# Kernel optimization log

Measured on AMD Instinct MI355X. Metric: run time of the kernel, lower is better.

The kernel has to match this reference:

```python
import jax, jax.numpy as jnp
import numpy as np

B, N = 65536, 8
OBS0, OBS1, OBS2 = 6, 1024, 7
H, HC, NA = 64, 128, 2


def _glorot(key, shape):
    fan_in = shape[0]
    lim = 1.0 / np.sqrt(fan_in)
    return jax.random.uniform(key, shape, jnp.float32, -lim, lim)


def setup_inputs() -> dict:
    key = jax.random.key(0)
    ks = jax.random.split(key, 24)
    state0 = jax.random.normal(ks[0], (B, OBS0), jnp.float32)
    state1 = jax.random.normal(ks[1], (B, OBS1), jnp.float32)
    state2 = jax.random.normal(ks[2], (B, N, OBS2), jnp.float32)
    keep = (jax.random.uniform(ks[3], (B, N, 1)) > 0.35) | (jnp.arange(N)[None, :, None] == 0)
    state2 = state2 * keep.astype(jnp.float32)
    return {
        "state0": state0, "state1": state1, "state2": state2,
        "W0": _glorot(ks[4], (OBS0, H)), "b0": jnp.zeros((H,), jnp.float32),
        "Wg": _glorot(ks[5], (OBS1, H)), "bg": jnp.zeros((H,), jnp.float32),
        "Ws1": _glorot(ks[6], (OBS2, H)), "bs1": jnp.zeros((H,), jnp.float32),
        "Ws2": _glorot(ks[7], (H, H)), "bs2": jnp.zeros((H,), jnp.float32),
        "Wq": _glorot(ks[8], (H, H)),
        "Wk": _glorot(ks[9], (H, H)),
        "Wv": _glorot(ks[10], (H, H)),
        "Wc1": _glorot(ks[11], (3 * H, HC)), "bc1": jnp.zeros((HC,), jnp.float32),
        "Wc2": _glorot(ks[12], (HC, HC)), "bc2": jnp.zeros((HC,), jnp.float32),
        "Wc3": _glorot(ks[13], (HC, NA)), "bc3": jnp.zeros((NA,), jnp.float32),
    }


def reference(state0, state1, state2,
              W0, b0, Wg, bg, Ws1, bs1, Ws2, bs2,
              Wq, Wk, Wv, Wc1, bc1, Wc2, bc2, Wc3, bc3):
    own_e = jax.nn.relu(state0 @ W0 + b0)                      # [B, 64]
    env_e = jax.nn.relu(state1 @ Wg + bg)                      # [B, 64]
    intru_e = jax.nn.relu(state2 @ Ws1 + bs1)                  # [B, N, 64]
    intru_e = jax.nn.relu(intru_e @ Ws2 + bs2)                 # [B, N, 64]

    q = own_e @ Wq                                             # [B, 64]
    k = intru_e @ Wk                                           # [B, N, 64]
    v = intru_e @ Wv                                           # [B, N, 64]

    # mask: True where the neighbor slot is non-padding (mean over feats != 0)
    mask = jnp.mean(state2, axis=2, keepdims=True) != 0        # [B, N, 1] bool

    score = jnp.einsum('bnd,bd->bn', k, q)[..., None]          # [B, N, 1]
    score_m = jnp.where(mask, score, -jnp.inf)
    alpha = jax.nn.softmax(score_m / np.sqrt(H), axis=1)       # [B, N, 1]
    alpha_m = jnp.where(mask, alpha, 0.0)
    v_att = jnp.sum(v * alpha_m, axis=1)                       # [B, 64]

    concat = jnp.concatenate((own_e, env_e, v_att), axis=1)    # [B, 192]
    h = jax.nn.relu(concat @ Wc1 + bc1)
    h = jax.nn.relu(h @ Wc2 + bc2)
    return jnp.tanh(h @ Wc3 + bc3)                             # [B, n_actions]
```

## Files before the change

kernel.cpp:

```cpp
#include <hip/hip_runtime.h>
#include <math.h>


typedef float f32x4 __attribute__((ext_vector_type(4)));
typedef float f32x4u __attribute__((ext_vector_type(4), aligned(4)));
typedef float f32x2u __attribute__((ext_vector_type(2), aligned(4)));
typedef __bf16 bf16x8 __attribute__((ext_vector_type(8)));
typedef unsigned short u16x8 __attribute__((ext_vector_type(8)));

#define DI __device__ __forceinline__

DI unsigned short f2bf_u(float f) {
  unsigned u = __builtin_bit_cast(unsigned, f);
  u += 0x7fffu + ((u >> 16) & 1u);
  return (unsigned short)(u >> 16);
}
DI float bfu2f(unsigned short s) {
  unsigned u = ((unsigned)s) << 16;
  return __builtin_bit_cast(float, u);
}
DI u16x8 cvt8(f32x4 x, f32x4 y) {
  bf16x8 r;
  r[0] = (__bf16)x[0]; r[1] = (__bf16)x[1]; r[2] = (__bf16)x[2]; r[3] = (__bf16)x[3];
  r[4] = (__bf16)y[0]; r[5] = (__bf16)y[1]; r[6] = (__bf16)y[2]; r[7] = (__bf16)y[3];
  return __builtin_bit_cast(u16x8, r);
}
DI f32x4 mfma16(u16x8 a, u16x8 b, f32x4 c) {
  return __builtin_amdgcn_mfma_f32_16x16x32_bf16(
      __builtin_bit_cast(bf16x8, a), __builtin_bit_cast(bf16x8, b), c, 0, 0, 0);
}


constexpr size_t WS_WGF = 0;
constexpr size_t WS_WS2 = 131072;
constexpr size_t WS_WV  = 139264;
constexpr size_t WS_MQK = 147456;
constexpr size_t WS_WC1 = 155648;
constexpr size_t WS_WC2 = 204800;
constexpr size_t WS_ENV = 237568;

__global__ __launch_bounds__(256) void k_prep(
    const float* __restrict__ Wg, const float* __restrict__ Ws2,
    const float* __restrict__ Wv, const float* __restrict__ Wq,
    const float* __restrict__ Wk, const float* __restrict__ Wc1,
    const float* __restrict__ Wc2,
    unsigned short* __restrict__ wgf, unsigned short* __restrict__ ws2f,
    unsigned short* __restrict__ wvf, unsigned short* __restrict__ mqkf,
    unsigned short* __restrict__ wc1f, unsigned short* __restrict__ wc2f) {
  const int idx = blockIdx.x * 256 + threadIdx.x;
  const float* src = nullptr;
  unsigned short* dst;
  int i, ntm, NC;
  bool is_mqk = false;
  if (idx < 65536)      { src = Wg;  dst = wgf;  i = idx;          ntm = 2; NC = 64;  }
  else if (idx < 69632) { src = Ws2; dst = ws2f; i = idx - 65536;  ntm = 2; NC = 64;  }
  else if (idx < 73728) { src = Wv;  dst = wvf;  i = idx - 69632;  ntm = 2; NC = 64;  }
  else if (idx < 77824) { is_mqk = true; dst = mqkf; i = idx - 73728; ntm = 2; NC = 64; }
  else if (idx < 102400){ src = Wc1; dst = wc1f; i = idx - 77824;  ntm = 3; NC = 128; }
  else                  { src = Wc2; dst = wc2f; i = idx - 102400; ntm = 3; NC = 128; }
  const int j = i & 7, ln = (i >> 3) & 63, t2 = i >> 9;
  const int nt = t2 & ((1 << ntm) - 1), kt = t2 >> ntm;
  const int k = kt * 32 + (ln >> 4) * 8 + j, n = nt * 16 + (ln & 15);
  float val;
  if (is_mqk) {
    const f32x4* qp = (const f32x4*)(Wq + k * 64);
    const f32x4* kp = (const f32x4*)(Wk + n * 64);
    float acc = 0.f;
#pragma unroll
    for (int d4 = 0; d4 < 16; ++d4) {
      const f32x4 a = qp[d4], b = kp[d4];
#pragma unroll
      for (int e = 0; e < 4; ++e) acc = fmaf(a[e], b[e], acc);
    }
    val = acc;
  } else {
    val = src[k * NC + n];
  }
  dst[i] = f2bf_u(val);
}

__global__ __launch_bounds__(256, 3) void k_env(
    const float* __restrict__ s1, const float* __restrict__ bg,
    const unsigned short* __restrict__ wgf, unsigned short* __restrict__ env) {
  __shared__ __align__(16) f32x4 RED[16 * 64];
  const int tid = threadIdx.x, lane = tid & 63, wave = tid >> 6;
  const int lo = lane & 15, q = lane >> 4;
  const int r0 = blockIdx.x * 16;
  const float* arow = s1 + (size_t)(r0 + lo) * 1024 + wave * 256 + q * 8;

  f32x4 A[8][2];
#pragma unroll
  for (int ks = 0; ks < 8; ++ks) {
    A[ks][0] = *(const f32x4*)(arow + ks * 32);
    A[ks][1] = *(const f32x4*)(arow + ks * 32 + 4);
  }
  const u16x8* wp = (const u16x8*)wgf + lane;
  u16x8 Bb[2][4];
#pragma unroll
  for (int nt = 0; nt < 4; ++nt) Bb[0][nt] = wp[((wave * 8) * 4 + nt) * 64];
  f32x4 acc[4] = {};
#pragma unroll
  for (int ks = 0; ks < 8; ++ks) {
    const int cur = ks & 1;
    if (ks < 7) {
#pragma unroll
      for (int nt = 0; nt < 4; ++nt)
        Bb[cur ^ 1][nt] = wp[((wave * 8 + ks + 1) * 4 + nt) * 64];
    }
    const u16x8 af = cvt8(A[ks][0], A[ks][1]);
#pragma unroll
    for (int nt = 0; nt < 4; ++nt) acc[nt] = mfma16(af, Bb[cur][nt], acc[nt]);
  }
#pragma unroll
  for (int nt = 0; nt < 4; ++nt) RED[(wave * 4 + nt) * 64 + lane] = acc[nt];
  __syncthreads();
  f32x4 s = RED[(0 * 4 + wave) * 64 + lane];
#pragma unroll
  for (int p = 1; p < 4; ++p) s += RED[(p * 4 + wave) * 64 + lane];
  const float bias = bg[wave * 16 + lo];
#pragma unroll
  for (int ri = 0; ri < 4; ++ri)
    env[(size_t)(r0 + q * 4 + ri) * 64 + wave * 16 + lo] =
        f2bf_u(fmaxf(s[ri] + bias, 0.f));
}

__global__ __launch_bounds__(256, 3) void k_rest(
    const float* __restrict__ s0, const float* __restrict__ s2,
    const unsigned short* __restrict__ env,
    const float* __restrict__ W0, const float* __restrict__ b0v,
    const float* __restrict__ Ws1, const float* __restrict__ bs1,
    const unsigned short* __restrict__ ws2f, const float* __restrict__ bs2,
    const unsigned short* __restrict__ wvf, const unsigned short* __restrict__ mqkf,
    const unsigned short* __restrict__ wc1f, const float* __restrict__ bc1,
    const unsigned short* __restrict__ wc2f, const float* __restrict__ bc2,
    const float* __restrict__ Wc3, const float* __restrict__ bc3,
    float* __restrict__ out) {
  __shared__ __align__(16) char smem[53248];
  u16x8* EF = (u16x8*)smem;
  unsigned short* EFs = (unsigned short*)smem;
  u16x8* H1F = (u16x8*)smem;
  unsigned short* H1Fs = (unsigned short*)smem;
  float* H2 = (float*)(smem + 8192);
  u16x8* CF = (u16x8*)(smem + 32768);
  unsigned short* CFs = (unsigned short*)(smem + 32768);
  float* SC = (float*)(smem + 36864);
  float* QK = (float*)(smem + 45056);
  u16x8* SEF = (u16x8*)(smem + 45056);

  const int tid = threadIdx.x;
  const int lane = tid & 63, wave = tid >> 6;
  const int lo = lane & 15, q = lane >> 4;
  const int bbase = blockIdx.x * 32;

  const int bl8 = tid >> 3, n8 = tid & 7;
  const float* s2p = s2 + ((size_t)(bbase + bl8) * 8 + n8) * 7;
  const f32x4u x03 = *(const f32x4u*)s2p;
  const f32x2u x45 = *(const f32x2u*)(s2p + 4);
  const float x6 = s2p[6];
  const float* s0p = s0 + (size_t)(bbase + bl8) * 6;
  const f32x4u y03 = *(const f32x4u*)s0p;
  const f32x2u y45 = *(const f32x2u*)(s0p + 4);
  const u16x8 ev = *(const u16x8*)(env + (size_t)(bbase + bl8) * 64 + n8 * 8);

  bool maskreg;
  {
    float xv[7] = {x03[0], x03[1], x03[2], x03[3], x45[0], x45[1], x6};
    const float sum = xv[0] + xv[1] + xv[2] + xv[3] + xv[4] + xv[5] + xv[6];
    maskreg = (sum != 0.f);
    const int mt = tid >> 4, rl = tid & 15;
#pragma unroll
    for (int c = 0; c < 8; ++c) {
      float a[8];
#pragma unroll
      for (int i = 0; i < 8; ++i) a[i] = bs1[c * 8 + i];
#pragma unroll
      for (int j = 0; j < 7; ++j) {
        const float* wr = Ws1 + j * 64 + c * 8;
#pragma unroll
        for (int i = 0; i < 8; ++i) a[i] = fmaf(xv[j], wr[i], a[i]);
      }
      u16x8 pk;
#pragma unroll
      for (int i = 0; i < 8; ++i) pk[i] = f2bf_u(fmaxf(a[i], 0.f));
      EF[(mt * 2 + (c >> 2)) * 64 + (((c & 3) << 4) | rl)] = pk;
    }
  }
  __syncthreads();

  {
    u16x8 Bf[4][2];
#pragma unroll
    for (int nt = 0; nt < 4; ++nt)
#pragma unroll
      for (int kt = 0; kt < 2; ++kt)
        Bf[nt][kt] = ((const u16x8*)ws2f)[(kt * 4 + nt) * 64 + lane];
    float bias[4];
#pragma unroll
    for (int nt = 0; nt < 4; ++nt) bias[nt] = bs2[nt * 16 + lo];
#pragma unroll
    for (int mi = 0; mi < 4; ++mi) {
      const int mt = wave * 4 + mi;
      const u16x8 A0 = EF[(mt * 2 + 0) * 64 + lane];
      const u16x8 A1 = EF[(mt * 2 + 1) * 64 + lane];
      f32x4 acc[4] = {};
#pragma unroll
      for (int nt = 0; nt < 4; ++nt) {
        acc[nt] = mfma16(A0, Bf[nt][0], acc[nt]);
        acc[nt] = mfma16(A1, Bf[nt][1], acc[nt]);
      }
#pragma unroll
      for (int nt = 0; nt < 4; ++nt) {
        const int h = nt * 16 + lo;
#pragma unroll
        for (int ri = 0; ri < 4; ++ri) {
          const float v = fmaxf(acc[nt][ri] + bias[nt], 0.f);
          const int rr = mt * 16 + q * 4 + ri;
          EFs[((mt * 2 + (h >> 5)) * 64 + ((((h >> 3) & 3) << 4) | (rr & 15))) * 8 +
              (h & 7)] = f2bf_u(v);
        }
      }
    }
  }
  __syncthreads();

  {
    const int mt = bl8 >> 4, fl = ((n8 & 3) << 4) | (bl8 & 15), kt = n8 >> 2;
    const float yv[6] = {y03[0], y03[1], y03[2], y03[3], y45[0], y45[1]};
    float a[8];
#pragma unroll
    for (int i = 0; i < 8; ++i) a[i] = b0v[n8 * 8 + i];
#pragma unroll
    for (int j = 0; j < 6; ++j) {
      const float* wr = W0 + j * 64 + n8 * 8;
#pragma unroll
      for (int i = 0; i < 8; ++i) a[i] = fmaf(yv[j], wr[i], a[i]);
    }
    u16x8 pk;
#pragma unroll
    for (int i = 0; i < 8; ++i) pk[i] = f2bf_u(fmaxf(a[i], 0.f));
    CF[(mt * 6 + kt) * 64 + fl] = pk;
    CF[(mt * 6 + 2 + kt) * 64 + fl] = ev;
  }
  __syncthreads();

  {
#pragma unroll
    for (int pp = 0; pp < 2; ++pp) {
      const int pr = wave * 2 + pp, mt = pr >> 2, nt = pr & 3;
      const u16x8 A0 = CF[(mt * 6 + 0) * 64 + lane];
      const u16x8 A1 = CF[(mt * 6 + 1) * 64 + lane];
      const u16x8 B0 = ((const u16x8*)mqkf)[(0 * 4 + nt) * 64 + lane];
      const u16x8 B1 = ((const u16x8*)mqkf)[(1 * 4 + nt) * 64 + lane];
      f32x4 acc = {};
      acc = mfma16(A0, B0, acc);
      acc = mfma16(A1, B1, acc);
#pragma unroll
      for (int ri = 0; ri < 4; ++ri)
        QK[(mt * 16 + q * 4 + ri) * 64 + nt * 16 + lo] = acc[ri];
    }
  }
  __syncthreads();

  {
    const int r = tid, bl = r >> 3, mt = r >> 4, rl = r & 15;
    float dot = 0.f;
#pragma unroll
    for (int c = 0; c < 8; ++c) {
      const u16x8 e = EF[(mt * 2 + (c >> 2)) * 64 + (((c & 3) << 4) | rl)];
      const float* qkp = QK + bl * 64 + c * 8;
      const f32x4 qa = *(const f32x4*)(qkp);
      const f32x4 qb = *(const f32x4*)(qkp + 4);
#pragma unroll
      for (int i = 0; i < 4; ++i) dot = fmaf(bfu2f(e[i]), qa[i], dot);
#pragma unroll
      for (int i = 0; i < 4; ++i) dot = fmaf(bfu2f(e[4 + i]), qb[i], dot);
    }
    SC[r] = maskreg ? dot * 0.125f : -1e30f;
  }
  __syncthreads();

  if (tid < 32) {
    float s[8];
#pragma unroll
    for (int n = 0; n < 8; ++n) s[n] = SC[tid * 8 + n];
    float mx = s[0];
#pragma unroll
    for (int n = 1; n < 8; ++n) mx = fmaxf(mx, s[n]);
    float e[8], sum = 0.f;
#pragma unroll
    for (int n = 0; n < 8; ++n) { e[n] = __expf(s[n] - mx); sum += e[n]; }
    const float inv = 1.f / sum;
#pragma unroll
    for (int n = 0; n < 8; ++n) SC[tid * 8 + n] = e[n] * inv;
  }
  __syncthreads();

  {
    float al[8];
#pragma unroll
    for (int n = 0; n < 8; ++n) al[n] = SC[bl8 * 8 + n];
    float a[8] = {0.f, 0.f, 0.f, 0.f, 0.f, 0.f, 0.f, 0.f};
#pragma unroll
    for (int n = 0; n < 8; ++n) {
      const int rr = bl8 * 8 + n;
      const u16x8 e =
          EF[((rr >> 4) * 2 + (n8 >> 2)) * 64 + (((n8 & 3) << 4) | (rr & 15))];
#pragma unroll
      for (int i = 0; i < 8; ++i) a[i] = fmaf(al[n], bfu2f(e[i]), a[i]);
    }
    u16x8 pk;
#pragma unroll
    for (int i = 0; i < 8; ++i) pk[i] = f2bf_u(a[i]);
    SEF[((bl8 >> 4) * 2 + (n8 >> 2)) * 64 + (((n8 & 3) << 4) | (bl8 & 15))] = pk;
  }
  __syncthreads();

  {
#pragma unroll
    for (int pp = 0; pp < 2; ++pp) {
      const int pr = wave * 2 + pp, mt = pr >> 2, nt = pr & 3;
      const u16x8 A0 = SEF[(mt * 2 + 0) * 64 + lane];
      const u16x8 A1 = SEF[(mt * 2 + 1) * 64 + lane];
      const u16x8 B0 = ((const u16x8*)wvf)[(0 * 4 + nt) * 64 + lane];
      const u16x8 B1 = ((const u16x8*)wvf)[(1 * 4 + nt) * 64 + lane];
      f32x4 acc = {};
      acc = mfma16(A0, B0, acc);
      acc = mfma16(A1, B1, acc);
      const int h = nt * 16 + lo;
#pragma unroll
      for (int ri = 0; ri < 4; ++ri) {
        const int rr = mt * 16 + q * 4 + ri;
        CFs[((mt * 6 + 4 + (h >> 5)) * 64 + ((((h >> 3) & 3) << 4) | (rr & 15))) * 8 +
            (h & 7)] = f2bf_u(acc[ri]);
      }
    }
  }
  __syncthreads();

  {
    const int mt = wave & 1, ntb = (wave >> 1) * 4;
    u16x8 A[6];
#pragma unroll
    for (int kt = 0; kt < 6; ++kt) A[kt] = CF[(mt * 6 + kt) * 64 + lane];
#pragma unroll
    for (int ni = 0; ni < 4; ++ni) {
      const int nt = ntb + ni;
      f32x4 acc = {};
#pragma unroll
      for (int kt = 0; kt < 6; ++kt) {
        const u16x8 Bf = ((const u16x8*)wc1f)[(kt * 8 + nt) * 64 + lane];
        acc = mfma16(A[kt], Bf, acc);
      }
      const float bias = bc1[nt * 16 + lo];
      const int h = nt * 16 + lo;
#pragma unroll
      for (int ri = 0; ri < 4; ++ri) {
        const float v = fmaxf(acc[ri] + bias, 0.f);
        const int rr = mt * 16 + q * 4 + ri;
        H1Fs[((mt * 4 + (h >> 5)) * 64 + ((((h >> 3) & 3) << 4) | (rr & 15))) * 8 +
             (h & 7)] = f2bf_u(v);
      }
    }
  }
  __syncthreads();

  {
    const int mt = wave & 1, ntb = (wave >> 1) * 4;
    u16x8 A[4];
#pragma unroll
    for (int kt = 0; kt < 4; ++kt) A[kt] = H1F[(mt * 4 + kt) * 64 + lane];
#pragma unroll
    for (int ni = 0; ni < 4; ++ni) {
      const int nt = ntb + ni;
      f32x4 acc = {};
#pragma unroll
      for (int kt = 0; kt < 4; ++kt) {
        const u16x8 Bf = ((const u16x8*)wc2f)[(kt * 8 + nt) * 64 + lane];
        acc = mfma16(A[kt], Bf, acc);
      }
      const float bias = bc2[nt * 16 + lo];
#pragma unroll
      for (int ri = 0; ri < 4; ++ri)
        H2[(mt * 16 + q * 4 + ri) * 132 + nt * 16 + lo] =
            fmaxf(acc[ri] + bias, 0.f);
    }
  }
  __syncthreads();

  {
    const int kq = n8 >> 1, a = n8 & 1;
    const f32x4* h4 = (const f32x4*)(H2 + bl8 * 132 + kq * 32);
    const float* wr = Wc3 + kq * 64;
    float acc = 0.f;
#pragma unroll
    for (int j4 = 0; j4 < 8; ++j4) {
      const f32x4 hv = h4[j4];
#pragma unroll
      for (int e = 0; e < 4; ++e) acc = fmaf(hv[e], wr[(j4 * 4 + e) * 2 + a], acc);
    }
    acc += __shfl_down(acc, 2);
    acc += __shfl_down(acc, 4);
    if (kq == 0) out[(size_t)(bbase + bl8) * 2 + a] = tanhf(acc + bc3[a]);
  }
}

extern "C" void kernel_launch(void* const* d_in, const int* in_sizes, int n_in,
                              void* d_out, int out_size, void* d_ws, size_t ws_size,
                              hipStream_t stream) {
  const float* s0  = (const float*)d_in[0];
  const float* s1  = (const float*)d_in[1];
  const float* s2  = (const float*)d_in[2];
  const float* W0  = (const float*)d_in[3];
  const float* b0  = (const float*)d_in[4];
  const float* Wg  = (const float*)d_in[5];
  const float* bg  = (const float*)d_in[6];
  const float* Ws1 = (const float*)d_in[7];
  const float* bs1 = (const float*)d_in[8];
  const float* Ws2 = (const float*)d_in[9];
  const float* bs2 = (const float*)d_in[10];
  const float* Wq  = (const float*)d_in[11];
  const float* Wk  = (const float*)d_in[12];
  const float* Wv  = (const float*)d_in[13];
  const float* Wc1 = (const float*)d_in[14];
  const float* bc1 = (const float*)d_in[15];
  const float* Wc2 = (const float*)d_in[16];
  const float* bc2 = (const float*)d_in[17];
  const float* Wc3 = (const float*)d_in[18];
  const float* bc3 = (const float*)d_in[19];

  char* ws = (char*)d_ws;
  unsigned short* wgf  = (unsigned short*)(ws + WS_WGF);
  unsigned short* ws2f = (unsigned short*)(ws + WS_WS2);
  unsigned short* wvf  = (unsigned short*)(ws + WS_WV);
  unsigned short* mqkf = (unsigned short*)(ws + WS_MQK);
  unsigned short* wc1f = (unsigned short*)(ws + WS_WC1);
  unsigned short* wc2f = (unsigned short*)(ws + WS_WC2);
  unsigned short* env  = (unsigned short*)(ws + WS_ENV);

  hipLaunchKernelGGL(k_prep, dim3(464), dim3(256), 0, stream, Wg, Ws2, Wv, Wq,
                     Wk, Wc1, Wc2, wgf, ws2f, wvf, mqkf, wc1f, wc2f);
  hipLaunchKernelGGL(k_env, dim3(4096), dim3(256), 0, stream, s1, bg, wgf, env);
  hipLaunchKernelGGL(k_rest, dim3(2048), dim3(256), 0, stream, s0, s2, env, W0,
                     b0, Ws1, bs1, ws2f, bs2, wvf, mqkf, wc1f, bc1, wc2f, bc2,
                     Wc3, bc3, (float*)d_out);
}
```

Measured before the change: 469.5 us.

## Fuse env GEMM into main kernel with 16-row blocks

Merges the state1 projection kernel into the main per-row kernel, so the env embedding no longer takes a round trip through global memory in bf16 and one kernel launch disappears. Each block now handles 16 batch rows instead of 32, and every later stage is remapped to that smaller tile. Shared memory is repacked into a smaller footprint and launch bounds raised so more blocks fit per CU. The state1 loads are split into two halves, with the second half prefetched during the first MFMAs. In exchange, each block carries more serial stages and syncs per row, and several later stages leave half the threads idle.

```diff
diff --git a/kernel.cpp b/kernel.cpp
--- a/kernel.cpp
+++ b/kernel.cpp
@@ -37,7 +37,6 @@
 constexpr size_t WS_MQK = 147456;
 constexpr size_t WS_WC1 = 155648;
 constexpr size_t WS_WC2 = 204800;
-constexpr size_t WS_ENV = 237568;
 
 __global__ __launch_bounds__(256) void k_prep(
     const float* __restrict__ Wg, const float* __restrict__ Ws2,
@@ -79,97 +78,74 @@
   dst[i] = f2bf_u(val);
 }
 
-__global__ __launch_bounds__(256, 3) void k_env(
-    const float* __restrict__ s1, const float* __restrict__ bg,
-    const unsigned short* __restrict__ wgf, unsigned short* __restrict__ env) {
-  __shared__ __align__(16) f32x4 RED[16 * 64];
-  const int tid = threadIdx.x, lane = tid & 63, wave = tid >> 6;
-  const int lo = lane & 15, q = lane >> 4;
-  const int r0 = blockIdx.x * 16;
-  const float* arow = s1 + (size_t)(r0 + lo) * 1024 + wave * 256 + q * 8;
-
-  f32x4 A[8][2];
-#pragma unroll
-  for (int ks = 0; ks < 8; ++ks) {
-    A[ks][0] = *(const f32x4*)(arow + ks * 32);
-    A[ks][1] = *(const f32x4*)(arow + ks * 32 + 4);
-  }
-  const u16x8* wp = (const u16x8*)wgf + lane;
-  u16x8 Bb[2][4];
-#pragma unroll
-  for (int nt = 0; nt < 4; ++nt) Bb[0][nt] = wp[((wave * 8) * 4 + nt) * 64];
-  f32x4 acc[4] = {};
-#pragma unroll
-  for (int ks = 0; ks < 8; ++ks) {
-    const int cur = ks & 1;
-    if (ks < 7) {
-#pragma unroll
-      for (int nt = 0; nt < 4; ++nt)
-        Bb[cur ^ 1][nt] = wp[((wave * 8 + ks + 1) * 4 + nt) * 64];
-    }
-    const u16x8 af = cvt8(A[ks][0], A[ks][1]);
-#pragma unroll
-    for (int nt = 0; nt < 4; ++nt) acc[nt] = mfma16(af, Bb[cur][nt], acc[nt]);
-  }
-#pragma unroll
-  for (int nt = 0; nt < 4; ++nt) RED[(wave * 4 + nt) * 64 + lane] = acc[nt];
-  __syncthreads();
-  f32x4 s = RED[(0 * 4 + wave) * 64 + lane];
-#pragma unroll
-  for (int p = 1; p < 4; ++p) s += RED[(p * 4 + wave) * 64 + lane];
-  const float bias = bg[wave * 16 + lo];
-#pragma unroll
-  for (int ri = 0; ri < 4; ++ri)
-    env[(size_t)(r0 + q * 4 + ri) * 64 + wave * 16 + lo] =
-        f2bf_u(fmaxf(s[ri] + bias, 0.f));
-}
-
-__global__ __launch_bounds__(256, 3) void k_rest(
-    const float* __restrict__ s0, const float* __restrict__ s2,
-    const unsigned short* __restrict__ env,
+__global__ __launch_bounds__(256, 4) void k_main(
+    const float* __restrict__ s0, const float* __restrict__ s1,
+    const float* __restrict__ s2,
     const float* __restrict__ W0, const float* __restrict__ b0v,
+    const float* __restrict__ bg,
     const float* __restrict__ Ws1, const float* __restrict__ bs1,
     const unsigned short* __restrict__ ws2f, const float* __restrict__ bs2,
     const unsigned short* __restrict__ wvf, const unsigned short* __restrict__ mqkf,
     const unsigned short* __restrict__ wc1f, const float* __restrict__ bc1,
     const unsigned short* __restrict__ wc2f, const float* __restrict__ bc2,
     const float* __restrict__ Wc3, const float* __restrict__ bc3,
+    const unsigned short* __restrict__ wgf,
     float* __restrict__ out) {
-  __shared__ __align__(16) char smem[53248];
+  __shared__ __align__(16) char smem[39424];
   u16x8* EF = (u16x8*)smem;
   unsigned short* EFs = (unsigned short*)smem;
-  u16x8* H1F = (u16x8*)smem;
-  unsigned short* H1Fs = (unsigned short*)smem;
-  float* H2 = (float*)(smem + 8192);
-  u16x8* CF = (u16x8*)(smem + 32768);
-  unsigned short* CFs = (unsigned short*)(smem + 32768);
-  float* SC = (float*)(smem + 36864);
-  float* QK = (float*)(smem + 45056);
-  u16x8* SEF = (u16x8*)(smem + 45056);
+  u16x8* CF = (u16x8*)(smem + 16384);
+  unsigned short* CFs = (unsigned short*)(smem + 16384);
+  char* SCR = smem + 22528;
+  f32x4* RED4 = (f32x4*)SCR;
+  float* QK = (float*)SCR;
+  u16x8* SEF = (u16x8*)SCR;
+  u16x8* H1F = (u16x8*)SCR;
+  unsigned short* H1Fs = (unsigned short*)SCR;
+  float* H2 = (float*)(SCR + 4096);
+  float* SC = (float*)(smem + 38912);
 
   const int tid = threadIdx.x;
   const int lane = tid & 63, wave = tid >> 6;
   const int lo = lane & 15, q = lane >> 4;
-  const int bbase = blockIdx.x * 32;
-
-  const int bl8 = tid >> 3, n8 = tid & 7;
-  const float* s2p = s2 + ((size_t)(bbase + bl8) * 8 + n8) * 7;
+  const int bbase = blockIdx.x * 16;
+
+  const float* arow = s1 + (size_t)(bbase + lo) * 1024 + wave * 256 + q * 8;
+  f32x4 Ab0[4], Ab1[4];
+#pragma unroll
+  for (int i = 0; i < 4; ++i) {
+    Ab0[i] = *(const f32x4*)(arow + i * 32);
+    Ab1[i] = *(const f32x4*)(arow + i * 32 + 4);
+  }
+  const u16x8* wp = (const u16x8*)wgf + lane;
+  u16x8 Bb[2][4];
+#pragma unroll
+  for (int nt = 0; nt < 4; ++nt) Bb[0][nt] = wp[((wave * 8) * 4 + nt) * 64];
+
+  const int ir = tid >> 1, half = tid & 1;
+  const int ibl = ir >> 3, in_ = ir & 7;
+  const float* s2p = s2 + ((size_t)(bbase + ibl) * 8 + in_) * 7;
   const f32x4u x03 = *(const f32x4u*)s2p;
   const f32x2u x45 = *(const f32x2u*)(s2p + 4);
   const float x6 = s2p[6];
-  const float* s0p = s0 + (size_t)(bbase + bl8) * 6;
-  const f32x4u y03 = *(const f32x4u*)s0p;
-  const f32x2u y45 = *(const f32x2u*)(s0p + 4);
-  const u16x8 ev = *(const u16x8*)(env + (size_t)(bbase + bl8) * 64 + n8 * 8);
+  const int orow = tid >> 3, oc = tid & 7;
+  const float* s0p = s0 + (size_t)(bbase + orow) * 6;
+  f32x4u y03 = {};
+  f32x2u y45 = {};
+  if (tid < 128) {
+    y03 = *(const f32x4u*)s0p;
+    y45 = *(const f32x2u*)(s0p + 4);
+  }
 
   bool maskreg;
   {
     float xv[7] = {x03[0], x03[1], x03[2], x03[3], x45[0], x45[1], x6};
     const float sum = xv[0] + xv[1] + xv[2] + xv[3] + xv[4] + xv[5] + xv[6];
     maskreg = (sum != 0.f);
-    const int mt = tid >> 4, rl = tid & 15;
-#pragma unroll
-    for (int c = 0; c < 8; ++c) {
+    const int mt = ir >> 4, rl = ir & 15;
+#pragma unroll
+    for (int cc = 0; cc < 4; ++cc) {
+      const int c = half * 4 + cc;
       float a[8];
 #pragma unroll
       for (int i = 0; i < 8; ++i) a[i] = bs1[c * 8 + i];
@@ -182,10 +158,46 @@
       u16x8 pk;
 #pragma unroll
       for (int i = 0; i < 8; ++i) pk[i] = f2bf_u(fmaxf(a[i], 0.f));
-      EF[(mt * 2 + (c >> 2)) * 64 + (((c & 3) << 4) | rl)] = pk;
-    }
-  }
-  __syncthreads();
+      EF[(mt * 2 + half) * 64 + ((cc << 4) | rl)] = pk;
+    }
+  }
+
+  {
+    f32x4 acc[4] = {};
+#pragma unroll
+    for (int ks = 0; ks < 8; ++ks) {
+      const int cur = ks & 1;
+      if (ks < 7) {
+#pragma unroll
+        for (int nt = 0; nt < 4; ++nt)
+          Bb[cur ^ 1][nt] = wp[((wave * 8 + ks + 1) * 4 + nt) * 64];
+      }
+      const u16x8 af = cvt8(Ab0[ks & 3], Ab1[ks & 3]);
+      if (ks < 4) {
+        Ab0[ks] = *(const f32x4*)(arow + (ks + 4) * 32);
+        Ab1[ks] = *(const f32x4*)(arow + (ks + 4) * 32 + 4);
+      }
+#pragma unroll
+      for (int nt = 0; nt < 4; ++nt) acc[nt] = mfma16(af, Bb[cur][nt], acc[nt]);
+    }
+#pragma unroll
+    for (int nt = 0; nt < 4; ++nt) RED4[(wave * 4 + nt) * 64 + lane] = acc[nt];
+  }
+  __syncthreads();
+
+  {
+    f32x4 s = RED4[(0 * 4 + wave) * 64 + lane];
+#pragma unroll
+    for (int pp = 1; pp < 4; ++pp) s += RED4[(pp * 4 + wave) * 64 + lane];
+    const float bias = bg[wave * 16 + lo];
+    const int h = wave * 16 + lo;
+#pragma unroll
+    for (int ri = 0; ri < 4; ++ri) {
+      const float v = fmaxf(s[ri] + bias, 0.f);
+      CFs[((2 + (h >> 5)) * 64 + ((((h >> 3) & 3) << 4) | (q * 4 + ri))) * 8 +
+          (h & 7)] = f2bf_u(v);
+    }
+  }
 
   {
     u16x8 Bf[4][2];
@@ -198,8 +210,8 @@
 #pragma unroll
     for (int nt = 0; nt < 4; ++nt) bias[nt] = bs2[nt * 16 + lo];
 #pragma unroll
-    for (int mi = 0; mi < 4; ++mi) {
-      const int mt = wave * 4 + mi;
+    for (int mi = 0; mi < 2; ++mi) {
+      const int mt = wave * 2 + mi;
       const u16x8 A0 = EF[(mt * 2 + 0) * 64 + lane];
       const u16x8 A1 = EF[(mt * 2 + 1) * 64 + lane];
       f32x4 acc[4] = {};
@@ -221,53 +233,47 @@
       }
     }
   }
-  __syncthreads();
-
-  {
-    const int mt = bl8 >> 4, fl = ((n8 & 3) << 4) | (bl8 & 15), kt = n8 >> 2;
+
+  if (tid < 128) {
     const float yv[6] = {y03[0], y03[1], y03[2], y03[3], y45[0], y45[1]};
     float a[8];
 #pragma unroll
-    for (int i = 0; i < 8; ++i) a[i] = b0v[n8 * 8 + i];
+    for (int i = 0; i < 8; ++i) a[i] = b0v[oc * 8 + i];
 #pragma unroll
     for (int j = 0; j < 6; ++j) {
-      const float* wr = W0 + j * 64 + n8 * 8;
+      const float* wr = W0 + j * 64 + oc * 8;
 #pragma unroll
       for (int i = 0; i < 8; ++i) a[i] = fmaf(yv[j], wr[i], a[i]);
     }
     u16x8 pk;
 #pragma unroll
     for (int i = 0; i < 8; ++i) pk[i] = f2bf_u(fmaxf(a[i], 0.f));
-    CF[(mt * 6 + kt) * 64 + fl] = pk;
-    CF[(mt * 6 + 2 + kt) * 64 + fl] = ev;
-  }
-  __syncthreads();
-
-  {
-#pragma unroll
-    for (int pp = 0; pp < 2; ++pp) {
-      const int pr = wave * 2 + pp, mt = pr >> 2, nt = pr & 3;
-      const u16x8 A0 = CF[(mt * 6 + 0) * 64 + lane];
-      const u16x8 A1 = CF[(mt * 6 + 1) * 64 + lane];
-      const u16x8 B0 = ((const u16x8*)mqkf)[(0 * 4 + nt) * 64 + lane];
-      const u16x8 B1 = ((const u16x8*)mqkf)[(1 * 4 + nt) * 64 + lane];
-      f32x4 acc = {};
-      acc = mfma16(A0, B0, acc);
-      acc = mfma16(A1, B1, acc);
-#pragma unroll
-      for (int ri = 0; ri < 4; ++ri)
-        QK[(mt * 16 + q * 4 + ri) * 64 + nt * 16 + lo] = acc[ri];
-    }
-  }
-  __syncthreads();
-
-  {
-    const int r = tid, bl = r >> 3, mt = r >> 4, rl = r & 15;
+    CF[(oc >> 2) * 64 + (((oc & 3) << 4) | orow)] = pk;
+  }
+  __syncthreads();
+
+  {
+    const u16x8 A0 = CF[0 * 64 + lane];
+    const u16x8 A1 = CF[1 * 64 + lane];
+    const u16x8 B0 = ((const u16x8*)mqkf)[(0 * 4 + wave) * 64 + lane];
+    const u16x8 B1 = ((const u16x8*)mqkf)[(1 * 4 + wave) * 64 + lane];
+    f32x4 acc = {};
+    acc = mfma16(A0, B0, acc);
+    acc = mfma16(A1, B1, acc);
+#pragma unroll
+    for (int ri = 0; ri < 4; ++ri)
+      QK[(q * 4 + ri) * 64 + wave * 16 + lo] = acc[ri];
+  }
+  __syncthreads();
+
+  {
+    const int rl = ir & 15, mt = ir >> 4;
     float dot = 0.f;
 #pragma unroll
-    for (int c = 0; c < 8; ++c) {
-      const u16x8 e = EF[(mt * 2 + (c >> 2)) * 64 + (((c & 3) << 4) | rl)];
-      const float* qkp = QK + bl * 64 + c * 8;
+    for (int cc = 0; cc < 4; ++cc) {
+      const int c = half * 4 + cc;
+      const u16x8 e = EF[(mt * 2 + half) * 64 + ((cc << 4) | rl)];
+      const float* qkp = QK + ibl * 64 + c * 8;
       const f32x4 qa = *(const f32x4*)(qkp);
       const f32x4 qb = *(const f32x4*)(qkp + 4);
 #pragma unroll
@@ -275,11 +281,12 @@
 #pragma unroll
       for (int i = 0; i < 4; ++i) dot = fmaf(bfu2f(e[4 + i]), qb[i], dot);
     }
-    SC[r] = maskreg ? dot * 0.125f : -1e30f;
-  }
-  __syncthreads();
-
-  if (tid < 32) {
+    dot += __shfl_xor(dot, 1);
+    if (half == 0) SC[ir] = maskreg ? dot * 0.125f : -1e30f;
+  }
+  __syncthreads();
+
+  if (tid < 16) {
     float s[8];
 #pragma unroll
     for (int n = 0; n < 8; ++n) s[n] = SC[tid * 8 + n];
@@ -295,56 +302,52 @@
   }
   __syncthreads();
 
-  {
+  if (tid < 128) {
+    const int bl = tid >> 3, cch = tid & 7;
     float al[8];
 #pragma unroll
-    for (int n = 0; n < 8; ++n) al[n] = SC[bl8 * 8 + n];
+    for (int n = 0; n < 8; ++n) al[n] = SC[bl * 8 + n];
     float a[8] = {0.f, 0.f, 0.f, 0.f, 0.f, 0.f, 0.f, 0.f};
 #pragma unroll
     for (int n = 0; n < 8; ++n) {
-      const int rr = bl8 * 8 + n;
+      const int rr = bl * 8 + n;
       const u16x8 e =
-          EF[((rr >> 4) * 2 + (n8 >> 2)) * 64 + (((n8 & 3) << 4) | (rr & 15))];
+          EF[((rr >> 4) * 2 + (cch >> 2)) * 64 + (((cch & 3) << 4) | (rr & 15))];
 #pragma unroll
       for (int i = 0; i < 8; ++i) a[i] = fmaf(al[n], bfu2f(e[i]), a[i]);
     }
     u16x8 pk;
 #pragma unroll
     for (int i = 0; i < 8; ++i) pk[i] = f2bf_u(a[i]);
-    SEF[((bl8 >> 4) * 2 + (n8 >> 2)) * 64 + (((n8 & 3) << 4) | (bl8 & 15))] = pk;
-  }
-  __syncthreads();
-
-  {
-#pragma unroll
-    for (int pp = 0; pp < 2; ++pp) {
-      const int pr = wave * 2 + pp, mt = pr >> 2, nt = pr & 3;
-      const u16x8 A0 = SEF[(mt * 2 + 0) * 64 + lane];
-      const u16x8 A1 = SEF[(mt * 2 + 1) * 64 + lane];
-      const u16x8 B0 = ((const u16x8*)wvf)[(0 * 4 + nt) * 64 + lane];
-      const u16x8 B1 = ((const u16x8*)wvf)[(1 * 4 + nt) * 64 + lane];
-      f32x4 acc = {};
-      acc = mfma16(A0, B0, acc);
-      acc = mfma16(A1, B1, acc);
-      const int h = nt * 16 + lo;
-#pragma unroll
-      for (int ri = 0; ri < 4; ++ri) {
-        const int rr = mt * 16 + q * 4 + ri;
-        CFs[((mt * 6 + 4 + (h >> 5)) * 64 + ((((h >> 3) & 3) << 4) | (rr & 15))) * 8 +
-            (h & 7)] = f2bf_u(acc[ri]);
-      }
-    }
-  }
-  __syncthreads();
-
-  {
-    const int mt = wave & 1, ntb = (wave >> 1) * 4;
+    SEF[(cch >> 2) * 64 + (((cch & 3) << 4) | bl)] = pk;
+  }
+  __syncthreads();
+
+  {
+    const u16x8 A0 = SEF[0 * 64 + lane];
+    const u16x8 A1 = SEF[1 * 64 + lane];
+    const u16x8 B0 = ((const u16x8*)wvf)[(0 * 4 + wave) * 64 + lane];
+    const u16x8 B1 = ((const u16x8*)wvf)[(1 * 4 + wave) * 64 + lane];
+    f32x4 acc = {};
+    acc = mfma16(A0, B0, acc);
+    acc = mfma16(A1, B1, acc);
+    const int h = wave * 16 + lo;
+#pragma unroll
+    for (int ri = 0; ri < 4; ++ri) {
+      const int rr = q * 4 + ri;
+      CFs[((4 + (h >> 5)) * 64 + ((((h >> 3) & 3) << 4) | rr)) * 8 + (h & 7)] =
+          f2bf_u(acc[ri]);
+    }
+  }
+  __syncthreads();
+
+  {
     u16x8 A[6];
 #pragma unroll
-    for (int kt = 0; kt < 6; ++kt) A[kt] = CF[(mt * 6 + kt) * 64 + lane];
-#pragma unroll
-    for (int ni = 0; ni < 4; ++ni) {
-      const int nt = ntb + ni;
+    for (int kt = 0; kt < 6; ++kt) A[kt] = CF[kt * 64 + lane];
+#pragma unroll
+    for (int ni = 0; ni < 2; ++ni) {
+      const int nt = wave * 2 + ni;
       f32x4 acc = {};
 #pragma unroll
       for (int kt = 0; kt < 6; ++kt) {
@@ -356,22 +359,21 @@
 #pragma unroll
       for (int ri = 0; ri < 4; ++ri) {
         const float v = fmaxf(acc[ri] + bias, 0.f);
-        const int rr = mt * 16 + q * 4 + ri;
-        H1Fs[((mt * 4 + (h >> 5)) * 64 + ((((h >> 3) & 3) << 4) | (rr & 15))) * 8 +
-             (h & 7)] = f2bf_u(v);
-      }
-    }
-  }
-  __syncthreads();
-
-  {
-    const int mt = wave & 1, ntb = (wave >> 1) * 4;
+        const int rr = q * 4 + ri;
+        H1Fs[((h >> 5) * 64 + ((((h >> 3) & 3) << 4) | rr)) * 8 + (h & 7)] =
+            f2bf_u(v);
+      }
+    }
+  }
+  __syncthreads();
+
+  {
     u16x8 A[4];
 #pragma unroll
-    for (int kt = 0; kt < 4; ++kt) A[kt] = H1F[(mt * 4 + kt) * 64 + lane];
-#pragma unroll
-    for (int ni = 0; ni < 4; ++ni) {
-      const int nt = ntb + ni;
+    for (int kt = 0; kt < 4; ++kt) A[kt] = H1F[kt * 64 + lane];
+#pragma unroll
+    for (int ni = 0; ni < 2; ++ni) {
+      const int nt = wave * 2 + ni;
       f32x4 acc = {};
 #pragma unroll
       for (int kt = 0; kt < 4; ++kt) {
@@ -381,26 +383,26 @@
       const float bias = bc2[nt * 16 + lo];
 #pragma unroll
       for (int ri = 0; ri < 4; ++ri)
-        H2[(mt * 16 + q * 4 + ri) * 132 + nt * 16 + lo] =
-            fmaxf(acc[ri] + bias, 0.f);
-    }
-  }
-  __syncthreads();
-
-  {
-    const int kq = n8 >> 1, a = n8 & 1;
-    const f32x4* h4 = (const f32x4*)(H2 + bl8 * 132 + kq * 32);
-    const float* wr = Wc3 + kq * 64;
+        H2[(q * 4 + ri) * 132 + nt * 16 + lo] = fmaxf(acc[ri] + bias, 0.f);
+    }
+  }
+  __syncthreads();
+
+  {
+    const int row = tid >> 4, a = (tid >> 3) & 1, kseg = tid & 7;
+    const f32x4* h4 = (const f32x4*)(H2 + row * 132 + kseg * 16);
+    const float* wr = Wc3 + kseg * 32;
     float acc = 0.f;
 #pragma unroll
-    for (int j4 = 0; j4 < 8; ++j4) {
+    for (int j4 = 0; j4 < 4; ++j4) {
       const f32x4 hv = h4[j4];
 #pragma unroll
       for (int e = 0; e < 4; ++e) acc = fmaf(hv[e], wr[(j4 * 4 + e) * 2 + a], acc);
     }
+    acc += __shfl_down(acc, 1);
     acc += __shfl_down(acc, 2);
     acc += __shfl_down(acc, 4);
-    if (kq == 0) out[(size_t)(bbase + bl8) * 2 + a] = tanhf(acc + bc3[a]);
+    if (kseg == 0) out[(size_t)(bbase + row) * 2 + a] = tanhf(acc + bc3[a]);
   }
 }
 
@@ -435,12 +437,10 @@
   unsigned short* mqkf = (unsigned short*)(ws + WS_MQK);
   unsigned short* wc1f = (unsigned short*)(ws + WS_WC1);
   unsigned short* wc2f = (unsigned short*)(ws + WS_WC2);
-  unsigned short* env  = (unsigned short*)(ws + WS_ENV);
 
   hipLaunchKernelGGL(k_prep, dim3(464), dim3(256), 0, stream, Wg, Ws2, Wv, Wq,
                      Wk, Wc1, Wc2, wgf, ws2f, wvf, mqkf, wc1f, wc2f);
-  hipLaunchKernelGGL(k_env, dim3(4096), dim3(256), 0, stream, s1, bg, wgf, env);
-  hipLaunchKernelGGL(k_rest, dim3(2048), dim3(256), 0, stream, s0, s2, env, W0,
-                     b0, Ws1, bs1, ws2f, bs2, wvf, mqkf, wc1f, bc1, wc2f, bc2,
-                     Wc3, bc3, (float*)d_out);
-}
+  hipLaunchKernelGGL(k_main, dim3(4096), dim3(256), 0, stream, s0, s1, s2, W0,
+                     b0, bg, Ws1, bs1, ws2f, bs2, wvf, mqkf, wc1f, bc1, wc2f,
+                     bc2, Wc3, bc3, wgf, (float*)d_out);
+}
```

New measurement: 504.3 us. 1.07x slower.
